# Optimization experiments

Measured on AMD Instinct MI355X. Metric: run time of the kernel, lower is better.

Reference implementation:

```python
import jax, jax.numpy as jnp
import numpy as np
import math

NUM_HEADS = 16
HIDDEN = 1024
HEAD = HIDDEN // NUM_HEADS


def setup_inputs() -> dict:
    key = jax.random.key(0)
    ks = jax.random.split(key, 11)
    B, S, H = 2, 2048, HIDDEN
    s = 1.0 / math.sqrt(H)
    return {
        "q": jax.random.normal(ks[0], (B, S, H), jnp.float32),
        "k": jax.random.normal(ks[1], (B, S, H), jnp.float32),
        "v": jax.random.normal(ks[2], (B, S, H), jnp.float32),
        "Wq": jax.random.normal(ks[3], (H, H), jnp.float32) * s,
        "bq": jnp.zeros((H,), jnp.float32),
        "Wk": jax.random.normal(ks[4], (H, H), jnp.float32) * s,
        "bk": jnp.zeros((H,), jnp.float32),
        "Wv": jax.random.normal(ks[5], (H, H), jnp.float32) * s,
        "bv": jnp.zeros((H,), jnp.float32),
        "Wo": jax.random.normal(ks[6], (H, H), jnp.float32) * s,
        "bo": jnp.zeros((H,), jnp.float32),
    }


def reference(q, k, v, Wq, bq, Wk, bk, Wv, bv, Wo, bo):
    B, S, H = q.shape
    nh, hd = NUM_HEADS, HEAD
    # projections (torch Linear: x @ W.T + b)
    qp = (q @ Wq.T + bq).reshape(B, S, nh, hd).transpose(0, 2, 1, 3)  # [B,nh,S,hd]
    kp = (k @ Wk.T + bk).reshape(B, S, nh, hd).transpose(0, 2, 1, 3)
    vp = (v @ Wv.T + bv).reshape(B, S, nh, hd).transpose(0, 2, 1, 3)
    scores = jnp.einsum('bhqd,bhkd->bhqk', qp, kp) / math.sqrt(hd)
    attn = jax.nn.softmax(scores, axis=-1)  # [B,nh,S,S]
    o = jnp.einsum('bhqk,bhkd->bhqd', attn, vp)
    o = o.transpose(0, 2, 1, 3).reshape(B, S, H)
    return o @ Wo.T + bo
```

## Files before the change

### kernel.cpp

```cpp
#include <hip/hip_runtime.h>
#include <cstdint>
#include <type_traits>
#include <utility>

typedef __attribute__((ext_vector_type(8))) short short8;
typedef __attribute__((ext_vector_type(8))) _Float16 f16x8_t;
typedef __attribute__((ext_vector_type(4))) float f32x4;

template <typename V, typename = void>
struct mfma_h_takes : std::false_type {};
template <typename V>
struct mfma_h_takes<V, std::void_t<decltype(__builtin_amdgcn_mfma_f32_16x16x32_f16(
    std::declval<V>(), std::declval<V>(), std::declval<f32x4>(), 0, 0, 0))>>
    : std::true_type {};

using hfrag_t = std::conditional_t<mfma_h_takes<f16x8_t>::value, f16x8_t, short8>;
static_assert(mfma_h_takes<f16x8_t>::value || mfma_h_takes<short8>::value,
              "no usable mfma_f32_16x16x32_f16 signature");

__device__ __forceinline__ f32x4 mfma16h(hfrag_t a, hfrag_t b, f32x4 c) {
  return __builtin_amdgcn_mfma_f32_16x16x32_f16(a, b, c, 0, 0, 0);
}

__device__ __forceinline__ void gld_lds16(const void* g, void* l) {
  __builtin_amdgcn_global_load_lds(
      (const __attribute__((address_space(1))) void*)(uintptr_t)g,
      (__attribute__((address_space(3))) void*)(uint32_t)(uintptr_t)l, 16, 0, 0);
}

__device__ __forceinline__ uint16_t f16_rne(float x) {
  return __builtin_bit_cast(uint16_t, (_Float16)x);
}
__device__ __forceinline__ float f16_up(uint16_t h) {
  return (float)__builtin_bit_cast(_Float16, h);
}

__device__ __forceinline__ float exp2_fast(float x) {
#if __has_builtin(__builtin_amdgcn_exp2f)
  return __builtin_amdgcn_exp2f(x);
#else
  return exp2f(x);
#endif
}
__device__ __forceinline__ uint32_t pk_f16(float a, float b) {
#if __has_builtin(__builtin_amdgcn_cvt_pkrtz)
  return __builtin_bit_cast(uint32_t, __builtin_amdgcn_cvt_pkrtz(a, b));
#else
  union { uint16_t u[2]; uint32_t w; } r;
  r.u[0] = f16_rne(fminf(a, 65504.0f));
  r.u[1] = f16_rne(fminf(b, 65504.0f));
  return r.w;
#endif
}

__device__ __forceinline__ void lds_barrier() {
  asm volatile("s_waitcnt lgkmcnt(0)" ::: "memory");
  __builtin_amdgcn_sched_barrier(0);
  __builtin_amdgcn_s_barrier();
  __builtin_amdgcn_sched_barrier(0);
}

__device__ __forceinline__ int swz(int row, int col) {
  return row * 64 + ((((col >> 3) + row) & 7) << 3) + (col & 7);
}

struct SplitArgs {
  const float* src[7];
  uint16_t* hi[7];
  int n4[7];
};
__global__ void split_multi(SplitArgs a) {
  const int z = blockIdx.y;
  int i = blockIdx.x * 256 + threadIdx.x;
  if (i >= a.n4[z]) return;
  float4 x = ((const float4*)a.src[z])[i];
  ushort4 h;
  h.x = f16_rne(x.x);
  h.y = f16_rne(x.y);
  h.z = f16_rne(x.z);
  h.w = f16_rne(x.w);
  ((ushort4*)a.hi[z])[i] = h;
}

struct QKVArgs {
  const uint16_t* Ah[3];
  const uint16_t* Bh[3];
  const float* bias[3];
  uint16_t* oH[3];
};

__global__ __launch_bounds__(256, 3) void gemm_qkv(QKVArgs args) {
  __shared__ uint16_t lds[3][2][128][32];
  const int K = 1024;
  const int tid = threadIdx.x;
  const int wv = tid >> 6, lane = tid & 63;
  const int lm = lane & 15, g = lane >> 4;
  const int wm = (wv & 1) * 64, wn = (wv >> 1) * 64;
  const int z = blockIdx.z;
  const bool isT = (z == 2);
  const int t = blockIdx.x + 8 * blockIdx.y;
  const int kx = t & 7, j = t >> 3;
  const int sx = (j & 3) | ((kx & 1) << 2);
  const int sy = (j >> 2) | ((kx >> 1) << 3);
  const int gm0 = (isT ? sx : sy) * 128;
  const int gn0 = (isT ? sy : sx) * 128;

  const uint16_t* base[2] = {args.Ah[z] + (size_t)gm0 * K,
                             args.Bh[z] + (size_t)gn0 * K};
  const int rl = lane >> 2;
  const int scl = (((lane & 3) - (rl >> 1)) & 3) * 8;
  const int ucol = ((g + (lm >> 1)) & 3) * 8;

  f32x4 acc[4][4];
#pragma unroll
  for (int a = 0; a < 4; ++a)
#pragma unroll
    for (int b = 0; b < 4; ++b) acc[a][b] = (f32x4)0.0f;

#pragma unroll
  for (int jj = 0; jj < 4; ++jj) {
    const int c = wv + 4 * jj;
    const int p = c >> 3, r16 = (c & 7) * 16;
    gld_lds16(base[p] + (size_t)(r16 + rl) * K + 0 + scl, &lds[0][p][r16][0]);
  }

  int cur = 0, nxt = 1;
#pragma unroll 1
  for (int ti = 0; ti < 32; ++ti) {
    if (ti + 1 < 32) {
      const int kt = (ti + 1) * 32;
#pragma unroll
      for (int jj = 0; jj < 4; ++jj) {
        const int c = wv + 4 * jj;
        const int p = c >> 3, r16 = (c & 7) * 16;
        gld_lds16(base[p] + (size_t)(r16 + rl) * K + kt + scl,
                  &lds[nxt][p][r16][0]);
      }
      asm volatile("s_waitcnt vmcnt(4)" ::: "memory");
    } else {
      asm volatile("s_waitcnt vmcnt(0)" ::: "memory");
    }
    __builtin_amdgcn_sched_barrier(0);
    __builtin_amdgcn_s_barrier();
    __builtin_amdgcn_sched_barrier(0);
    hfrag_t af[4];
#pragma unroll
    for (int mf = 0; mf < 4; ++mf) {
      af[mf] = *(const hfrag_t*)&lds[cur][0][wm + mf * 16 + lm][ucol];
    }
#pragma unroll
    for (int nf = 0; nf < 4; ++nf) {
      hfrag_t bhf = *(const hfrag_t*)&lds[cur][1][wn + nf * 16 + lm][ucol];
#pragma unroll
      for (int mf = 0; mf < 4; ++mf) {
        acc[mf][nf] = mfma16h(af[mf], bhf, acc[mf][nf]);
      }
    }
    cur = nxt;
    nxt = nxt + 1;
    if (nxt == 3) nxt = 0;
  }
  const float* bias = args.bias[z];
  uint16_t* oH = args.oH[z];
  const float kQScale = 0.18033688f;
#pragma unroll
  for (int mf = 0; mf < 4; ++mf) {
#pragma unroll
    for (int nf = 0; nf < 4; ++nf) {
      const int col = gn0 + wn + nf * 16 + lm;
#pragma unroll
      for (int i = 0; i < 4; ++i) {
        const int row = gm0 + wm + mf * 16 + g * 4 + i;
        float v = acc[mf][nf][i] + (isT ? bias[row] : bias[col]);
        if (z == 0) v *= kQScale;
        size_t addr;
        if (!isT) {
          addr = ((size_t)((row >> 11) * 16 + (col >> 6)) * 2048 + (row & 2047)) * 64 +
                 (col & 63);
        } else {
          addr = ((size_t)((col >> 11) * 1024 + row)) * 2048 + (col & 2047);
        }
        oH[addr] = f16_rne(v);
      }
    }
  }
}

__global__ __launch_bounds__(256, 2) void gemm_o(
    const uint16_t* __restrict__ Ah, const uint16_t* __restrict__ Bh,
    const float* __restrict__ bias, float* __restrict__ out) {
  const int K = 1024, N = 1024;
  __shared__ uint16_t ldsA[2][64][64];
  __shared__ uint16_t ldsB[2][128][64];
  const int tid = threadIdx.x;
  const int wv = tid >> 6, lane = tid & 63;
  const int lm = lane & 15, g = lane >> 4;
  const int wm = (wv & 1) * 32, wn = (wv >> 1) * 64;
  const int t = blockIdx.x + 8 * blockIdx.y;
  const int kx = t & 7, j = t >> 3;
  const int sx = (j & 3) | ((kx & 1) << 2);
  const int sy = (j >> 2) | ((kx >> 1) << 4);
  const int gm0 = sy * 64, gn0 = sx * 128;
  const uint16_t* baseA = Ah + (size_t)gm0 * K;
  const uint16_t* baseB = Bh + (size_t)gn0 * K;
  const int rl8 = lane >> 3;
  const int scl = (((lane & 7) - rl8) & 7) * 8;

  f32x4 acc[2][4];
#pragma unroll
  for (int a = 0; a < 2; ++a)
#pragma unroll
    for (int b = 0; b < 4; ++b) acc[a][b] = (f32x4)0.0f;

#pragma unroll
  for (int jj = 0; jj < 6; ++jj) {
    const int c = wv + 4 * jj;
    if (c < 8) {
      gld_lds16(baseA + (size_t)(c * 8 + rl8) * K + 0 + scl, &ldsA[0][c * 8][0]);
    } else {
      const int b = c - 8;
      gld_lds16(baseB + (size_t)(b * 8 + rl8) * K + 0 + scl, &ldsB[0][b * 8][0]);
    }
  }

#pragma unroll 1
  for (int ti = 0; ti < 16; ++ti) {
    const int cur = ti & 1;
    if (ti + 1 < 16) {
      const int kt = (ti + 1) * 64;
#pragma unroll
      for (int jj = 0; jj < 6; ++jj) {
        const int c = wv + 4 * jj;
        if (c < 8) {
          gld_lds16(baseA + (size_t)(c * 8 + rl8) * K + kt + scl,
                    &ldsA[cur ^ 1][c * 8][0]);
        } else {
          const int b = c - 8;
          gld_lds16(baseB + (size_t)(b * 8 + rl8) * K + kt + scl,
                    &ldsB[cur ^ 1][b * 8][0]);
        }
      }
      asm volatile("s_waitcnt vmcnt(6)" ::: "memory");
    } else {
      asm volatile("s_waitcnt vmcnt(0)" ::: "memory");
    }
    __builtin_amdgcn_sched_barrier(0);
    __builtin_amdgcn_s_barrier();
    __builtin_amdgcn_sched_barrier(0);
#pragma unroll
    for (int ks = 0; ks < 2; ++ks) {
      const int uc = ((ks * 4 + g + lm) & 7) * 8;
      hfrag_t af[2];
#pragma unroll
      for (int mf = 0; mf < 2; ++mf) {
        af[mf] = *(const hfrag_t*)&ldsA[cur][wm + mf * 16 + lm][uc];
      }
#pragma unroll
      for (int nf = 0; nf < 4; ++nf) {
        hfrag_t bhf = *(const hfrag_t*)&ldsB[cur][wn + nf * 16 + lm][uc];
#pragma unroll
        for (int mf = 0; mf < 2; ++mf) {
          acc[mf][nf] = mfma16h(af[mf], bhf, acc[mf][nf]);
        }
      }
    }
    __builtin_amdgcn_sched_barrier(0);
    __builtin_amdgcn_s_barrier();
    __builtin_amdgcn_sched_barrier(0);
  }
#pragma unroll
  for (int mf = 0; mf < 2; ++mf)
#pragma unroll
    for (int nf = 0; nf < 4; ++nf) {
      const int col = gn0 + wn + nf * 16 + lm;
#pragma unroll
      for (int i = 0; i < 4; ++i) {
        const int row = gm0 + wm + mf * 16 + g * 4 + i;
        out[(size_t)row * N + col] = acc[mf][nf][i] + bias[col];
      }
    }
}

__global__ __launch_bounds__(256, 2) void attn_kernel(
    const uint16_t* __restrict__ Qh,
    const uint16_t* __restrict__ Kh,
    const uint16_t* __restrict__ Vh,
    float* __restrict__ opart, float* __restrict__ lpart) {
  __shared__ uint16_t kt[4096];
  __shared__ uint16_t vt[4096];
  __shared__ uint16_t pp[8192];
  const int tid = threadIdx.x;
  const int wave = tid >> 6, lane = tid & 63;
  const int lm = lane & 15, g = lane >> 4;
  const int linear = blockIdx.x + 32 * blockIdx.y;
  const int bh = (linear & 7) + 8 * (linear >> 8);
  const int qt = (linear >> 3) & 15;
  const int half = (linear >> 7) & 1;
  const int kvh = half * 1024;
  const size_t base = (size_t)bh * 131072;
  const int q0 = qt * 128 + wave * 32;

  hfrag_t qf[2][2];
#pragma unroll
  for (int b = 0; b < 2; ++b) {
    const size_t rb = base + (size_t)(q0 + b * 16 + lm) * 64 + g * 8;
    qf[b][0] = *(const hfrag_t*)(Qh + rb);
    qf[b][1] = *(const hfrag_t*)(Qh + rb + 32);
  }
  f32x4 oacc[2][4];
  f32x4 lacc[2];
#pragma unroll
  for (int mf = 0; mf < 2; ++mf) {
    lacc[mf] = (f32x4)0.0f;
#pragma unroll
    for (int nf = 0; nf < 4; ++nf) oacc[mf][nf] = (f32x4)0.0f;
  }
  short8 ones_s = (short8)(short)0x3C00;
  hfrag_t ones = __builtin_bit_cast(hfrag_t, ones_s);

  const int sr = tid >> 3;
  const int sc = (tid & 7) * 8;

  uint4 kr0, kr1, vr0, vr1;
  {
    const size_t ka = base + (size_t)(kvh + sr) * 64 + sc;
    kr0 = *(const uint4*)(Kh + ka);
    kr1 = *(const uint4*)(Kh + ka + 2048);
  }

#pragma unroll 1
  for (int it = 0; it < 16; ++it) {
    const int kv0 = kvh + it * 64;
    *(uint4*)&kt[swz(sr, sc)] = kr0;
    *(uint4*)&kt[swz(sr + 32, sc)] = kr1;
    lds_barrier();
    {
      const size_t va = base + (size_t)sr * 2048 + kv0 + sc;
      vr0 = *(const uint4*)(Vh + va);
      vr1 = *(const uint4*)(Vh + va + 65536);
    }
    if (it + 1 < 16) {
      const size_t ka = base + (size_t)(kv0 + 64 + sr) * 64 + sc;
      kr0 = *(const uint4*)(Kh + ka);
      kr1 = *(const uint4*)(Kh + ka + 2048);
    }
    f32x4 sct[4][2];
#pragma unroll
    for (int a = 0; a < 4; ++a)
#pragma unroll
      for (int b = 0; b < 2; ++b) sct[a][b] = (f32x4)0.0f;
    __builtin_amdgcn_s_setprio(1);
#pragma unroll
    for (int ks = 0; ks < 2; ++ks) {
#pragma unroll
      for (int a = 0; a < 4; ++a) {
        hfrag_t kfh = *(const hfrag_t*)&kt[swz(a * 16 + lm, ks * 32 + g * 8)];
#pragma unroll
        for (int b = 0; b < 2; ++b) {
          sct[a][b] = mfma16h(kfh, qf[b][ks], sct[a][b]);
        }
      }
    }
    __builtin_amdgcn_s_setprio(0);
#pragma unroll
    for (int a = 0; a < 4; ++a) {
#pragma unroll
      for (int b = 0; b < 2; ++b) {
        float e0 = exp2_fast(sct[a][b][0]);
        float e1 = exp2_fast(sct[a][b][1]);
        float e2 = exp2_fast(sct[a][b][2]);
        float e3 = exp2_fast(sct[a][b][3]);
        uint2 pk;
        pk.x = pk_f16(e0, e1);
        pk.y = pk_f16(e2, e3);
        *(uint2*)&pp[swz(wave * 32 + b * 16 + lm, a * 16 + g * 4)] = pk;
      }
    }
    *(uint4*)&vt[swz(sr, sc)] = vr0;
    *(uint4*)&vt[swz(sr + 32, sc)] = vr1;
    lds_barrier();
    __builtin_amdgcn_s_setprio(1);
#pragma unroll
    for (int ks = 0; ks < 2; ++ks) {
      hfrag_t pa[2];
#pragma unroll
      for (int mf = 0; mf < 2; ++mf) {
        pa[mf] = *(const hfrag_t*)&pp[swz(wave * 32 + mf * 16 + lm, ks * 32 + g * 8)];
        lacc[mf] = mfma16h(pa[mf], ones, lacc[mf]);
      }
#pragma unroll
      for (int nf = 0; nf < 4; ++nf) {
        hfrag_t vbh = *(const hfrag_t*)&vt[swz(nf * 16 + lm, ks * 32 + g * 8)];
#pragma unroll
        for (int mf = 0; mf < 2; ++mf) {
          oacc[mf][nf] = mfma16h(pa[mf], vbh, oacc[mf][nf]);
        }
      }
    }
    __builtin_amdgcn_s_setprio(0);
  }
  const int obase = (half * 32 + bh) * 2048;
#pragma unroll
  for (int mf = 0; mf < 2; ++mf) {
#pragma unroll
    for (int i = 0; i < 4; ++i) {
      const int qrow = qt * 128 + wave * 32 + mf * 16 + g * 4 + i;
      float* orow = opart + ((size_t)obase + qrow) * 64;
#pragma unroll
      for (int nf = 0; nf < 4; ++nf) orow[nf * 16 + lm] = oacc[mf][nf][i];
      if (lm == 0) lpart[obase + qrow] = lacc[mf][i];
    }
  }
}

__global__ void combine_kernel(const float* __restrict__ opart,
                               const float* __restrict__ lpart,
                               uint16_t* __restrict__ oh) {
  const int idx = blockIdx.x * 256 + threadIdx.x;
  const float4 a = ((const float4*)opart)[idx];
  const float4 b = ((const float4*)(opart + 4194304))[idx];
  const int row = idx >> 4;
  const float linv = 1.0f / (lpart[row] + lpart[65536 + row]);
  const int bh = row >> 11, qq = row & 2047;
  const int bb = bh >> 4, hh = bh & 15;
  const size_t o = ((size_t)(bb * 2048 + qq)) * 1024 + hh * 64 + (idx & 15) * 4;
  ushort4 H;
  H.x = f16_rne((a.x + b.x) * linv);
  H.y = f16_rne((a.y + b.y) * linv);
  H.z = f16_rne((a.z + b.z) * linv);
  H.w = f16_rne((a.w + b.w) * linv);
  *(ushort4*)(oh + o) = H;
}

extern "C" void kernel_launch(void* const* d_in, const int* in_sizes, int n_in,
                              void* d_out, int out_size, void* d_ws, size_t ws_size,
                              hipStream_t stream) {
  const float* q = (const float*)d_in[0];
  const float* k = (const float*)d_in[1];
  const float* v = (const float*)d_in[2];
  const float* Wq = (const float*)d_in[3];
  const float* bq = (const float*)d_in[4];
  const float* Wk = (const float*)d_in[5];
  const float* bk = (const float*)d_in[6];
  const float* Wv = (const float*)d_in[7];
  const float* bv = (const float*)d_in[8];
  const float* Wo = (const float*)d_in[9];
  const float* bo = (const float*)d_in[10];

  const size_t NX = 4194304;
  const size_t NW = 1048576;
  uint16_t* p = (uint16_t*)d_ws;
  uint16_t* xqh = p; p += NX; uint16_t* xql = p; p += NX;
  uint16_t* xkh = p; p += NX; uint16_t* xkl = p; p += NX;
  uint16_t* xvh = p; p += NX; uint16_t* xvl = p; p += NX;
  uint16_t* wqh = p; p += NW; uint16_t* wql = p; p += NW;
  uint16_t* wkh = p; p += NW; uint16_t* wkl = p; p += NW;
  uint16_t* wvh = p; p += NW; uint16_t* wvl = p; p += NW;
  uint16_t* woh = p; p += NW; uint16_t* wol = p; p += NW;
  uint16_t* qph = p; p += NX; uint16_t* qpl = p; p += NX;
  uint16_t* kph = p; p += NX; uint16_t* kpl = p; p += NX;
  uint16_t* vth = p; p += NX; uint16_t* vtl = p; p += NX;
  uint16_t* oh = xqh;
  float* opart = (float*)xkh;
  float* lpart = opart + 2 * 4194304;

  SplitArgs sa;
  sa.src[0] = q;  sa.hi[0] = xqh; sa.n4[0] = (int)(NX / 4);
  sa.src[1] = k;  sa.hi[1] = xkh; sa.n4[1] = (int)(NX / 4);
  sa.src[2] = v;  sa.hi[2] = xvh; sa.n4[2] = (int)(NX / 4);
  sa.src[3] = Wq; sa.hi[3] = wqh; sa.n4[3] = (int)(NW / 4);
  sa.src[4] = Wk; sa.hi[4] = wkh; sa.n4[4] = (int)(NW / 4);
  sa.src[5] = Wv; sa.hi[5] = wvh; sa.n4[5] = (int)(NW / 4);
  sa.src[6] = Wo; sa.hi[6] = woh; sa.n4[6] = (int)(NW / 4);
  split_multi<<<dim3((unsigned)(NX / 4 / 256), 7), 256, 0, stream>>>(sa);

  QKVArgs qa;
  qa.Ah[0] = xqh; qa.Bh[0] = wqh; qa.bias[0] = bq; qa.oH[0] = qph;
  qa.Ah[1] = xkh; qa.Bh[1] = wkh; qa.bias[1] = bk; qa.oH[1] = kph;
  qa.Ah[2] = wvh; qa.Bh[2] = xvh; qa.bias[2] = bv; qa.oH[2] = vth;
  gemm_qkv<<<dim3(8, 32, 3), 256, 0, stream>>>(qa);

  attn_kernel<<<dim3(32, 32), 256, 0, stream>>>(qph, kph, vth, opart, lpart);
  combine_kernel<<<4096, 256, 0, stream>>>(opart, lpart, oh);

  gemm_o<<<dim3(8, 64), 256, 0, stream>>>(oh, woh, bo, (float*)d_out);
}
```

Before: 233.5 us.

## Fuse split-KV combine into attention via last-block-done atomic flags

Removes the separate combine kernel. Each attention block still writes its partial output and row sums, then atomically bumps a per-(head, q-tile) counter. The second block to arrive reads the other half's partials, merges them with its own in-register accumulators, normalises and writes the fp16 output. The flags are zeroed inside the existing split kernel. This saves one kernel launch and one pass that re-read both partials, at the cost of an atomic, a fence and extra syncs per block. It still writes the redundant partials and adds a cross-block memory-ordering dependency.

Result: slower. 259.2 us (+11.0%).

```diff
diff --git a/kernel.cpp b/kernel.cpp
--- a/kernel.cpp
+++ b/kernel.cpp
@@ -67,11 +67,16 @@
 struct SplitArgs {
   const float* src[7];
   uint16_t* hi[7];
+  uint32_t* flags;
   int n4[7];
 };
 __global__ void split_multi(SplitArgs a) {
   const int z = blockIdx.y;
   int i = blockIdx.x * 256 + threadIdx.x;
+  if (z == 0 && blockIdx.x == 0) {
+    a.flags[threadIdx.x] = 0;
+    a.flags[threadIdx.x + 256] = 0;
+  }
   if (i >= a.n4[z]) return;
   float4 x = ((const float4*)a.src[z])[i];
   ushort4 h;
@@ -285,10 +290,12 @@
     const uint16_t* __restrict__ Qh,
     const uint16_t* __restrict__ Kh,
     const uint16_t* __restrict__ Vh,
-    float* __restrict__ opart, float* __restrict__ lpart) {
+    float* __restrict__ opart, float* __restrict__ lpart,
+    uint32_t* __restrict__ flags, uint16_t* __restrict__ oh) {
   __shared__ uint16_t kt[4096];
   __shared__ uint16_t vt[4096];
   __shared__ uint16_t pp[8192];
+  __shared__ int role;
   const int tid = threadIdx.x;
   const int wave = tid >> 6, lane = tid & 63;
   const int lm = lane & 15, g = lane >> 4;
@@ -411,25 +418,32 @@
       if (lm == 0) lpart[obase + qrow] = lacc[mf][i];
     }
   }
-}
-
-__global__ void combine_kernel(const float* __restrict__ opart,
-                               const float* __restrict__ lpart,
-                               uint16_t* __restrict__ oh) {
-  const int idx = blockIdx.x * 256 + threadIdx.x;
-  const float4 a = ((const float4*)opart)[idx];
-  const float4 b = ((const float4*)(opart + 4194304))[idx];
-  const int row = idx >> 4;
-  const float linv = 1.0f / (lpart[row] + lpart[65536 + row]);
-  const int bh = row >> 11, qq = row & 2047;
-  const int bb = bh >> 4, hh = bh & 15;
-  const size_t o = ((size_t)(bb * 2048 + qq)) * 1024 + hh * 64 + (idx & 15) * 4;
-  ushort4 H;
-  H.x = f16_rne((a.x + b.x) * linv);
-  H.y = f16_rne((a.y + b.y) * linv);
-  H.z = f16_rne((a.z + b.z) * linv);
-  H.w = f16_rne((a.w + b.w) * linv);
-  *(ushort4*)(oh + o) = H;
+  __syncthreads();
+  if (tid == 0) {
+    __threadfence();
+    role = (int)atomicAdd(&flags[bh * 16 + qt], 1u);
+  }
+  __syncthreads();
+  if (role == 1) {
+    const int obase2 = ((1 - half) * 32 + bh) * 2048;
+    const size_t dbase = ((size_t)(bh >> 4) * 2048) * 1024 + (size_t)(bh & 15) * 64;
+#pragma unroll
+    for (int mf = 0; mf < 2; ++mf) {
+#pragma unroll
+      for (int i = 0; i < 4; ++i) {
+        const int qrow = qt * 128 + wave * 32 + mf * 16 + g * 4 + i;
+        const float lsum = lacc[mf][i] + lpart[obase2 + qrow];
+        const float linv = 1.0f / lsum;
+        const float* orow = opart + ((size_t)obase2 + qrow) * 64;
+        uint16_t* dst = oh + dbase + (size_t)qrow * 1024;
+#pragma unroll
+        for (int nf = 0; nf < 4; ++nf) {
+          float v = (oacc[mf][nf][i] + orow[nf * 16 + lm]) * linv;
+          dst[nf * 16 + lm] = f16_rne(v);
+        }
+      }
+    }
+  }
 }
 
 extern "C" void kernel_launch(void* const* d_in, const int* in_sizes, int n_in,
@@ -460,6 +474,7 @@
   uint16_t* qph = p; p += NX; uint16_t* qpl = p; p += NX;
   uint16_t* kph = p; p += NX; uint16_t* kpl = p; p += NX;
   uint16_t* vth = p; p += NX; uint16_t* vtl = p; p += NX;
+  uint32_t* flags = (uint32_t*)p;
   uint16_t* oh = xqh;
   float* opart = (float*)xkh;
   float* lpart = opart + 2 * 4194304;
@@ -472,6 +487,7 @@
   sa.src[4] = Wk; sa.hi[4] = wkh; sa.n4[4] = (int)(NW / 4);
   sa.src[5] = Wv; sa.hi[5] = wvh; sa.n4[5] = (int)(NW / 4);
   sa.src[6] = Wo; sa.hi[6] = woh; sa.n4[6] = (int)(NW / 4);
+  sa.flags = flags;
   split_multi<<<dim3((unsigned)(NX / 4 / 256), 7), 256, 0, stream>>>(sa);
 
   QKVArgs qa;
@@ -480,8 +496,8 @@
   qa.Ah[2] = wvh; qa.Bh[2] = xvh; qa.bias[2] = bv; qa.oH[2] = vth;
   gemm_qkv<<<dim3(8, 32, 3), 256, 0, stream>>>(qa);
 
-  attn_kernel<<<dim3(32, 32), 256, 0, stream>>>(qph, kph, vth, opart, lpart);
-  combine_kernel<<<4096, 256, 0, stream>>>(opart, lpart, oh);
+  attn_kernel<<<dim3(32, 32), 256, 0, stream>>>(qph, kph, vth, opart, lpart,
+                                                flags, oh);
 
   gemm_o<<<dim3(8, 64), 256, 0, stream>>>(oh, woh, bo, (float*)d_out);
 }
```

## Double-buffer K/V in attention, split P per-wave phases, flatten split launch

Applied to the files above, without the earlier changes.

The attention loop now double-buffers the K and V tiles in LDS and prefetches the next V tile alongside K. This removes the second block-wide barrier per iteration, so P@V uses wave-local fences instead. The P tile is processed in two 32-column halves with a smaller swizzled buffer, cutting LDS use. The split kernel uses a flat 1D grid, so the many idle blocks launched for the smaller weight tensors are dropped. The cost is doubled K/V LDS, extra prefetch registers, and reliance on wave-local fences for correctness.

New measurement: 231.6 us. No clear change (-0.8%).

```diff
diff --git a/kernel.cpp b/kernel.cpp
--- a/kernel.cpp
+++ b/kernel.cpp
@@ -60,19 +60,36 @@
   __builtin_amdgcn_sched_barrier(0);
 }
 
+__device__ __forceinline__ void lds_fence_wave() {
+  asm volatile("s_waitcnt lgkmcnt(0)" ::: "memory");
+  __builtin_amdgcn_sched_barrier(0);
+}
+
 __device__ __forceinline__ int swz(int row, int col) {
   return row * 64 + ((((col >> 3) + row) & 7) << 3) + (col & 7);
+}
+
+__device__ __forceinline__ int ppidx(int row, int colf16) {
+  const int u = colf16 >> 3;
+  return row * 32 + (((u + row) & 3) << 3) + (colf16 & 7);
 }
 
 struct SplitArgs {
   const float* src[7];
   uint16_t* hi[7];
-  int n4[7];
 };
 __global__ void split_multi(SplitArgs a) {
-  const int z = blockIdx.y;
-  int i = blockIdx.x * 256 + threadIdx.x;
-  if (i >= a.n4[z]) return;
+  const int b = blockIdx.x;
+  int z, lb;
+  if (b < 12288) {
+    z = b >> 12;
+    lb = b & 4095;
+  } else {
+    const int r = b - 12288;
+    z = 3 + (r >> 10);
+    lb = r & 1023;
+  }
+  const int i = lb * 256 + threadIdx.x;
   float4 x = ((const float4*)a.src[z])[i];
   ushort4 h;
   h.x = f16_rne(x.x);
@@ -286,9 +303,9 @@
     const uint16_t* __restrict__ Kh,
     const uint16_t* __restrict__ Vh,
     float* __restrict__ opart, float* __restrict__ lpart) {
-  __shared__ uint16_t kt[4096];
-  __shared__ uint16_t vt[4096];
-  __shared__ uint16_t pp[8192];
+  __shared__ uint16_t kt[2][4096];
+  __shared__ uint16_t vt[2][4096];
+  __shared__ uint16_t pp[4096];
   const int tid = threadIdx.x;
   const int wave = tid >> 6, lane = tid & 63;
   const int lm = lane & 15, g = lane >> 4;
@@ -326,23 +343,27 @@
     const size_t ka = base + (size_t)(kvh + sr) * 64 + sc;
     kr0 = *(const uint4*)(Kh + ka);
     kr1 = *(const uint4*)(Kh + ka + 2048);
+    const size_t va = base + (size_t)sr * 2048 + kvh + sc;
+    vr0 = *(const uint4*)(Vh + va);
+    vr1 = *(const uint4*)(Vh + va + 65536);
   }
 
 #pragma unroll 1
   for (int it = 0; it < 16; ++it) {
+    const int cur = it & 1;
     const int kv0 = kvh + it * 64;
-    *(uint4*)&kt[swz(sr, sc)] = kr0;
-    *(uint4*)&kt[swz(sr + 32, sc)] = kr1;
+    *(uint4*)&kt[cur][swz(sr, sc)] = kr0;
+    *(uint4*)&kt[cur][swz(sr + 32, sc)] = kr1;
+    *(uint4*)&vt[cur][swz(sr, sc)] = vr0;
+    *(uint4*)&vt[cur][swz(sr + 32, sc)] = vr1;
     lds_barrier();
-    {
-      const size_t va = base + (size_t)sr * 2048 + kv0 + sc;
-      vr0 = *(const uint4*)(Vh + va);
-      vr1 = *(const uint4*)(Vh + va + 65536);
-    }
     if (it + 1 < 16) {
       const size_t ka = base + (size_t)(kv0 + 64 + sr) * 64 + sc;
       kr0 = *(const uint4*)(Kh + ka);
       kr1 = *(const uint4*)(Kh + ka + 2048);
+      const size_t va = base + (size_t)sr * 2048 + kv0 + 64 + sc;
+      vr0 = *(const uint4*)(Vh + va);
+      vr1 = *(const uint4*)(Vh + va + 65536);
     }
     f32x4 sct[4][2];
 #pragma unroll
@@ -354,7 +375,7 @@
     for (int ks = 0; ks < 2; ++ks) {
 #pragma unroll
       for (int a = 0; a < 4; ++a) {
-        hfrag_t kfh = *(const hfrag_t*)&kt[swz(a * 16 + lm, ks * 32 + g * 8)];
+        hfrag_t kfh = *(const hfrag_t*)&kt[cur][swz(a * 16 + lm, ks * 32 + g * 8)];
 #pragma unroll
         for (int b = 0; b < 2; ++b) {
           sct[a][b] = mfma16h(kfh, qf[b][ks], sct[a][b]);
@@ -363,41 +384,41 @@
     }
     __builtin_amdgcn_s_setprio(0);
 #pragma unroll
-    for (int a = 0; a < 4; ++a) {
-#pragma unroll
-      for (int b = 0; b < 2; ++b) {
-        float e0 = exp2_fast(sct[a][b][0]);
-        float e1 = exp2_fast(sct[a][b][1]);
-        float e2 = exp2_fast(sct[a][b][2]);
-        float e3 = exp2_fast(sct[a][b][3]);
-        uint2 pk;
-        pk.x = pk_f16(e0, e1);
-        pk.y = pk_f16(e2, e3);
-        *(uint2*)&pp[swz(wave * 32 + b * 16 + lm, a * 16 + g * 4)] = pk;
-      }
-    }
-    *(uint4*)&vt[swz(sr, sc)] = vr0;
-    *(uint4*)&vt[swz(sr + 32, sc)] = vr1;
-    lds_barrier();
-    __builtin_amdgcn_s_setprio(1);
-#pragma unroll
-    for (int ks = 0; ks < 2; ++ks) {
+    for (int ph = 0; ph < 2; ++ph) {
+#pragma unroll
+      for (int a2 = 0; a2 < 2; ++a2) {
+        const int a = ph * 2 + a2;
+#pragma unroll
+        for (int b = 0; b < 2; ++b) {
+          float e0 = exp2_fast(sct[a][b][0]);
+          float e1 = exp2_fast(sct[a][b][1]);
+          float e2 = exp2_fast(sct[a][b][2]);
+          float e3 = exp2_fast(sct[a][b][3]);
+          uint2 pk;
+          pk.x = pk_f16(e0, e1);
+          pk.y = pk_f16(e2, e3);
+          *(uint2*)&pp[ppidx(wave * 32 + b * 16 + lm, a2 * 16 + g * 4)] = pk;
+        }
+      }
+      lds_fence_wave();
+      __builtin_amdgcn_s_setprio(1);
       hfrag_t pa[2];
 #pragma unroll
       for (int mf = 0; mf < 2; ++mf) {
-        pa[mf] = *(const hfrag_t*)&pp[swz(wave * 32 + mf * 16 + lm, ks * 32 + g * 8)];
+        pa[mf] = *(const hfrag_t*)&pp[ppidx(wave * 32 + mf * 16 + lm, g * 8)];
         lacc[mf] = mfma16h(pa[mf], ones, lacc[mf]);
       }
 #pragma unroll
       for (int nf = 0; nf < 4; ++nf) {
-        hfrag_t vbh = *(const hfrag_t*)&vt[swz(nf * 16 + lm, ks * 32 + g * 8)];
+        hfrag_t vbh = *(const hfrag_t*)&vt[cur][swz(nf * 16 + lm, ph * 32 + g * 8)];
 #pragma unroll
         for (int mf = 0; mf < 2; ++mf) {
           oacc[mf][nf] = mfma16h(pa[mf], vbh, oacc[mf][nf]);
         }
       }
-    }
-    __builtin_amdgcn_s_setprio(0);
+      __builtin_amdgcn_s_setprio(0);
+      lds_fence_wave();
+    }
   }
   const int obase = (half * 32 + bh) * 2048;
 #pragma unroll
@@ -465,14 +486,14 @@
   float* lpart = opart + 2 * 4194304;
 
   SplitArgs sa;
-  sa.src[0] = q;  sa.hi[0] = xqh; sa.n4[0] = (int)(NX / 4);
-  sa.src[1] = k;  sa.hi[1] = xkh; sa.n4[1] = (int)(NX / 4);
-  sa.src[2] = v;  sa.hi[2] = xvh; sa.n4[2] = (int)(NX / 4);
-  sa.src[3] = Wq; sa.hi[3] = wqh; sa.n4[3] = (int)(NW / 4);
-  sa.src[4] = Wk; sa.hi[4] = wkh; sa.n4[4] = (int)(NW / 4);
-  sa.src[5] = Wv; sa.hi[5] = wvh; sa.n4[5] = (int)(NW / 4);
-  sa.src[6] = Wo; sa.hi[6] = woh; sa.n4[6] = (int)(NW / 4);
-  split_multi<<<dim3((unsigned)(NX / 4 / 256), 7), 256, 0, stream>>>(sa);
+  sa.src[0] = q;  sa.hi[0] = xqh;
+  sa.src[1] = k;  sa.hi[1] = xkh;
+  sa.src[2] = v;  sa.hi[2] = xvh;
+  sa.src[3] = Wq; sa.hi[3] = wqh;
+  sa.src[4] = Wk; sa.hi[4] = wkh;
+  sa.src[5] = Wv; sa.hi[5] = wvh;
+  sa.src[6] = Wo; sa.hi[6] = woh;
+  split_multi<<<16384, 256, 0, stream>>>(sa);
 
   QKVArgs qa;
   qa.Ah[0] = xqh; qa.Bh[0] = wqh; qa.bias[0] = bq; qa.oH[0] = qph;
```

## Fuse split-KV combine into output projection GEMM and compact split launch

Applied to the files above, without the earlier changes.

Removes the separate combine kernel: gemm_o now reads both fp32 partial attention outputs plus the row sums, normalizes them, converts to fp16 and writes its A tile into LDS itself, so the fp16 intermediate is never written to and reread from global memory. The split kernel switches to a 1D grid with no idle blocks for the smaller weight tensors. The QKV GEMM goes from a triple-buffered LDS ring to double buffering with an extra barrier per iteration, which lowers LDS use. Each gemm_o block now recomputes the combine for its rows across all 8 column tiles, so partial outputs are read about 8 times and A loads become synchronous register loads rather than async LDS loads.

Result: no change. 230.8 us (-1.1%).

```diff
diff --git a/kernel.cpp b/kernel.cpp
--- a/kernel.cpp
+++ b/kernel.cpp
@@ -30,9 +30,6 @@
 
 __device__ __forceinline__ uint16_t f16_rne(float x) {
   return __builtin_bit_cast(uint16_t, (_Float16)x);
-}
-__device__ __forceinline__ float f16_up(uint16_t h) {
-  return (float)__builtin_bit_cast(_Float16, h);
 }
 
 __device__ __forceinline__ float exp2_fast(float x) {
@@ -67,12 +64,19 @@
 struct SplitArgs {
   const float* src[7];
   uint16_t* hi[7];
-  int n4[7];
 };
 __global__ void split_multi(SplitArgs a) {
-  const int z = blockIdx.y;
-  int i = blockIdx.x * 256 + threadIdx.x;
-  if (i >= a.n4[z]) return;
+  const int b = blockIdx.x;
+  int z, lb;
+  if (b < 12288) {
+    z = b >> 12;
+    lb = b & 4095;
+  } else {
+    const int r = b - 12288;
+    z = 3 + (r >> 10);
+    lb = r & 1023;
+  }
+  const int i = lb * 256 + threadIdx.x;
   float4 x = ((const float4*)a.src[z])[i];
   ushort4 h;
   h.x = f16_rne(x.x);
@@ -90,7 +94,7 @@
 };
 
 __global__ __launch_bounds__(256, 3) void gemm_qkv(QKVArgs args) {
-  __shared__ uint16_t lds[3][2][128][32];
+  __shared__ uint16_t lds[2][2][128][32];
   const int K = 1024;
   const int tid = threadIdx.x;
   const int wv = tid >> 6, lane = tid & 63;
@@ -124,9 +128,9 @@
     gld_lds16(base[p] + (size_t)(r16 + rl) * K + 0 + scl, &lds[0][p][r16][0]);
   }
 
-  int cur = 0, nxt = 1;
 #pragma unroll 1
   for (int ti = 0; ti < 32; ++ti) {
+    const int cur = ti & 1;
     if (ti + 1 < 32) {
       const int kt = (ti + 1) * 32;
 #pragma unroll
@@ -134,7 +138,7 @@
         const int c = wv + 4 * jj;
         const int p = c >> 3, r16 = (c & 7) * 16;
         gld_lds16(base[p] + (size_t)(r16 + rl) * K + kt + scl,
-                  &lds[nxt][p][r16][0]);
+                  &lds[cur ^ 1][p][r16][0]);
       }
       asm volatile("s_waitcnt vmcnt(4)" ::: "memory");
     } else {
@@ -156,9 +160,9 @@
         acc[mf][nf] = mfma16h(af[mf], bhf, acc[mf][nf]);
       }
     }
-    cur = nxt;
-    nxt = nxt + 1;
-    if (nxt == 3) nxt = 0;
+    __builtin_amdgcn_sched_barrier(0);
+    __builtin_amdgcn_s_barrier();
+    __builtin_amdgcn_sched_barrier(0);
   }
   const float* bias = args.bias[z];
   uint16_t* oH = args.oH[z];
@@ -187,8 +191,9 @@
 }
 
 __global__ __launch_bounds__(256, 2) void gemm_o(
-    const uint16_t* __restrict__ Ah, const uint16_t* __restrict__ Bh,
-    const float* __restrict__ bias, float* __restrict__ out) {
+    const float* __restrict__ opart, const float* __restrict__ lpart,
+    const uint16_t* __restrict__ Bh, const float* __restrict__ bias,
+    float* __restrict__ out) {
   const int K = 1024, N = 1024;
   __shared__ uint16_t ldsA[2][64][64];
   __shared__ uint16_t ldsB[2][128][64];
@@ -201,7 +206,6 @@
   const int sx = (j & 3) | ((kx & 1) << 2);
   const int sy = (j >> 2) | ((kx >> 1) << 4);
   const int gm0 = sy * 64, gn0 = sx * 128;
-  const uint16_t* baseA = Ah + (size_t)gm0 * K;
   const uint16_t* baseB = Bh + (size_t)gn0 * K;
   const int rl8 = lane >> 3;
   const int scl = (((lane & 7) - rl8) & 7) * 8;
@@ -213,14 +217,34 @@
     for (int b = 0; b < 4; ++b) acc[a][b] = (f32x4)0.0f;
 
 #pragma unroll
-  for (int jj = 0; jj < 6; ++jj) {
+  for (int jj = 0; jj < 4; ++jj) {
+    const int cb = wv + 4 * jj;
+    gld_lds16(baseB + (size_t)(cb * 8 + rl8) * K + 0 + scl, &ldsB[0][cb * 8][0]);
+  }
+#pragma unroll
+  for (int jj = 0; jj < 2; ++jj) {
     const int c = wv + 4 * jj;
-    if (c < 8) {
-      gld_lds16(baseA + (size_t)(c * 8 + rl8) * K + 0 + scl, &ldsA[0][c * 8][0]);
-    } else {
-      const int b = c - 8;
-      gld_lds16(baseB + (size_t)(b * 8 + rl8) * K + 0 + scl, &ldsB[0][b * 8][0]);
-    }
+    const int r = gm0 + c * 8 + rl8;
+    const int b = r >> 11, q = r & 2047;
+    const size_t li = (size_t)(b * 16 + 0) * 2048 + q;
+    const float* s0 = opart + li * 64 + scl;
+    float4 a0 = *(const float4*)s0;
+    float4 a1 = *(const float4*)(s0 + 4);
+    float4 b0 = *(const float4*)(s0 + 4194304);
+    float4 b1 = *(const float4*)(s0 + 4194304 + 4);
+    const float linv = 1.0f / (lpart[li] + lpart[li + 65536]);
+    ushort4 h0, h1;
+    h0.x = f16_rne((a0.x + b0.x) * linv);
+    h0.y = f16_rne((a0.y + b0.y) * linv);
+    h0.z = f16_rne((a0.z + b0.z) * linv);
+    h0.w = f16_rne((a0.w + b0.w) * linv);
+    h1.x = f16_rne((a1.x + b1.x) * linv);
+    h1.y = f16_rne((a1.y + b1.y) * linv);
+    h1.z = f16_rne((a1.z + b1.z) * linv);
+    h1.w = f16_rne((a1.w + b1.w) * linv);
+    ushort4* dst = (ushort4*)&ldsA[0][c * 8 + rl8][(lane & 7) * 8];
+    dst[0] = h0;
+    dst[1] = h1;
   }
 
 #pragma unroll 1
@@ -229,24 +253,16 @@
     if (ti + 1 < 16) {
       const int kt = (ti + 1) * 64;
 #pragma unroll
-      for (int jj = 0; jj < 6; ++jj) {
-        const int c = wv + 4 * jj;
-        if (c < 8) {
-          gld_lds16(baseA + (size_t)(c * 8 + rl8) * K + kt + scl,
-                    &ldsA[cur ^ 1][c * 8][0]);
-        } else {
-          const int b = c - 8;
-          gld_lds16(baseB + (size_t)(b * 8 + rl8) * K + kt + scl,
-                    &ldsB[cur ^ 1][b * 8][0]);
-        }
-      }
-      asm volatile("s_waitcnt vmcnt(6)" ::: "memory");
+      for (int jj = 0; jj < 4; ++jj) {
+        const int cb = wv + 4 * jj;
+        gld_lds16(baseB + (size_t)(cb * 8 + rl8) * K + kt + scl,
+                  &ldsB[cur ^ 1][cb * 8][0]);
+      }
+      asm volatile("s_waitcnt vmcnt(4)" ::: "memory");
     } else {
       asm volatile("s_waitcnt vmcnt(0)" ::: "memory");
     }
-    __builtin_amdgcn_sched_barrier(0);
-    __builtin_amdgcn_s_barrier();
-    __builtin_amdgcn_sched_barrier(0);
+    lds_barrier();
 #pragma unroll
     for (int ks = 0; ks < 2; ++ks) {
       const int uc = ((ks * 4 + g + lm) & 7) * 8;
@@ -264,9 +280,36 @@
         }
       }
     }
-    __builtin_amdgcn_sched_barrier(0);
-    __builtin_amdgcn_s_barrier();
-    __builtin_amdgcn_sched_barrier(0);
+    if (ti + 1 < 16) {
+      const int kt = (ti + 1) * 64;
+      const int h = kt >> 6;
+#pragma unroll
+      for (int jj = 0; jj < 2; ++jj) {
+        const int c = wv + 4 * jj;
+        const int r = gm0 + c * 8 + rl8;
+        const int b = r >> 11, q = r & 2047;
+        const size_t li = (size_t)(b * 16 + h) * 2048 + q;
+        const float* s0 = opart + li * 64 + scl;
+        float4 a0 = *(const float4*)s0;
+        float4 a1 = *(const float4*)(s0 + 4);
+        float4 b0 = *(const float4*)(s0 + 4194304);
+        float4 b1 = *(const float4*)(s0 + 4194304 + 4);
+        const float linv = 1.0f / (lpart[li] + lpart[li + 65536]);
+        ushort4 h0, h1;
+        h0.x = f16_rne((a0.x + b0.x) * linv);
+        h0.y = f16_rne((a0.y + b0.y) * linv);
+        h0.z = f16_rne((a0.z + b0.z) * linv);
+        h0.w = f16_rne((a0.w + b0.w) * linv);
+        h1.x = f16_rne((a1.x + b1.x) * linv);
+        h1.y = f16_rne((a1.y + b1.y) * linv);
+        h1.z = f16_rne((a1.z + b1.z) * linv);
+        h1.w = f16_rne((a1.w + b1.w) * linv);
+        ushort4* dst = (ushort4*)&ldsA[cur ^ 1][c * 8 + rl8][(lane & 7) * 8];
+        dst[0] = h0;
+        dst[1] = h1;
+      }
+    }
+    lds_barrier();
   }
 #pragma unroll
   for (int mf = 0; mf < 2; ++mf)
@@ -413,25 +456,6 @@
   }
 }
 
-__global__ void combine_kernel(const float* __restrict__ opart,
-                               const float* __restrict__ lpart,
-                               uint16_t* __restrict__ oh) {
-  const int idx = blockIdx.x * 256 + threadIdx.x;
-  const float4 a = ((const float4*)opart)[idx];
-  const float4 b = ((const float4*)(opart + 4194304))[idx];
-  const int row = idx >> 4;
-  const float linv = 1.0f / (lpart[row] + lpart[65536 + row]);
-  const int bh = row >> 11, qq = row & 2047;
-  const int bb = bh >> 4, hh = bh & 15;
-  const size_t o = ((size_t)(bb * 2048 + qq)) * 1024 + hh * 64 + (idx & 15) * 4;
-  ushort4 H;
-  H.x = f16_rne((a.x + b.x) * linv);
-  H.y = f16_rne((a.y + b.y) * linv);
-  H.z = f16_rne((a.z + b.z) * linv);
-  H.w = f16_rne((a.w + b.w) * linv);
-  *(ushort4*)(oh + o) = H;
-}
-
 extern "C" void kernel_launch(void* const* d_in, const int* in_sizes, int n_in,
                               void* d_out, int out_size, void* d_ws, size_t ws_size,
                               hipStream_t stream) {
@@ -460,19 +484,18 @@
   uint16_t* qph = p; p += NX; uint16_t* qpl = p; p += NX;
   uint16_t* kph = p; p += NX; uint16_t* kpl = p; p += NX;
   uint16_t* vth = p; p += NX; uint16_t* vtl = p; p += NX;
-  uint16_t* oh = xqh;
   float* opart = (float*)xkh;
   float* lpart = opart + 2 * 4194304;
 
   SplitArgs sa;
-  sa.src[0] = q;  sa.hi[0] = xqh; sa.n4[0] = (int)(NX / 4);
-  sa.src[1] = k;  sa.hi[1] = xkh; sa.n4[1] = (int)(NX / 4);
-  sa.src[2] = v;  sa.hi[2] = xvh; sa.n4[2] = (int)(NX / 4);
-  sa.src[3] = Wq; sa.hi[3] = wqh; sa.n4[3] = (int)(NW / 4);
-  sa.src[4] = Wk; sa.hi[4] = wkh; sa.n4[4] = (int)(NW / 4);
-  sa.src[5] = Wv; sa.hi[5] = wvh; sa.n4[5] = (int)(NW / 4);
-  sa.src[6] = Wo; sa.hi[6] = woh; sa.n4[6] = (int)(NW / 4);
-  split_multi<<<dim3((unsigned)(NX / 4 / 256), 7), 256, 0, stream>>>(sa);
+  sa.src[0] = q;  sa.hi[0] = xqh;
+  sa.src[1] = k;  sa.hi[1] = xkh;
+  sa.src[2] = v;  sa.hi[2] = xvh;
+  sa.src[3] = Wq; sa.hi[3] = wqh;
+  sa.src[4] = Wk; sa.hi[4] = wkh;
+  sa.src[5] = Wv; sa.hi[5] = wvh;
+  sa.src[6] = Wo; sa.hi[6] = woh;
+  split_multi<<<16384, 256, 0, stream>>>(sa);
 
   QKVArgs qa;
   qa.Ah[0] = xqh; qa.Bh[0] = wqh; qa.bias[0] = bq; qa.oH[0] = qph;
@@ -481,7 +504,6 @@
   gemm_qkv<<<dim3(8, 32, 3), 256, 0, stream>>>(qa);
 
   attn_kernel<<<dim3(32, 32), 256, 0, stream>>>(qph, kph, vth, opart, lpart);
-  combine_kernel<<<4096, 256, 0, stream>>>(opart, lpart, oh);
-
-  gemm_o<<<dim3(8, 64), 256, 0, stream>>>(oh, woh, bo, (float*)d_out);
-}
+
+  gemm_o<<<dim3(8, 64), 256, 0, stream>>>(opart, lpart, woh, bo, (float*)d_out);
+}
```
